# Kernel tuning notes

Hardware: AMD Instinct MI355X
Metric: run time of the kernel (lower is better)

Reference implementation:

```python
import jax, jax.numpy as jnp
import numpy as np

EPS = 1e-5


def setup_inputs() -> dict:
    key = jax.random.key(0)
    k1, k2, k3, k4 = jax.random.split(key, 4)
    N, E, D = 100000, 1600000, 128
    x = jax.random.normal(k1, (N, D), dtype=jnp.float32)
    weight = jax.random.normal(k2, (D, D), dtype=jnp.float32) * (1.0 / np.sqrt(D))
    bias = jnp.zeros((D,), dtype=jnp.float32)
    src = jax.random.randint(k3, (E,), 0, N, dtype=jnp.int32)
    dst = jax.random.randint(k4, (E,), 0, N, dtype=jnp.int32)
    return {"x": x, "weight": weight, "bias": bias, "src": src, "dst": dst}


def reference(x, weight, bias, src, dst):
    # GNNBasicBlock(layer_type='gcn', block_type='n_a_r', activation=('relu', False))
    N = x.shape[0]
    ones = jnp.ones(src.shape[0], dtype=x.dtype)
    # DGL GraphConv norm='both': D_out^{-1/2} on src side, D_in^{-1/2} on dst side,
    # degrees clamped to min 1.
    out_deg = jax.ops.segment_sum(ones, src, num_segments=N)
    in_deg = jax.ops.segment_sum(ones, dst, num_segments=N)
    norm_src = jnp.maximum(out_deg, 1.0) ** -0.5  # [N]
    norm_dst = jnp.maximum(in_deg, 1.0) ** -0.5   # [N]
    xs = x * norm_src[:, None]                    # [N, D]
    # gather src features per edge, sum-scatter to dst (aggregate first: in<=out)
    agg = jax.ops.segment_sum(xs[src], dst, num_segments=N)  # [E,D] -> [N,D]
    agg = agg * norm_dst[:, None]
    h = agg @ weight + bias                       # [N, D]
    # NodeNorm: per-node mean/var over feature dim, biased variance
    mean = jnp.mean(h, axis=1, keepdims=True)
    var = jnp.var(h, axis=1, keepdims=True)
    h = (h - mean) / jnp.sqrt(var + EPS)
    # relu + residual
    return jax.nn.relu(h) + x
```

## Files before the change

### kernel.cpp

```cpp
#include <hip/hip_runtime.h>

#define D 128
#define SPAN 64
#define NB_MAX 1600
#define CB 128
#define ECAP 1536

typedef __attribute__((ext_vector_type(8))) short short8;
typedef __attribute__((ext_vector_type(4))) float floatx4;
typedef __attribute__((ext_vector_type(4))) int   iv4;
typedef __attribute__((ext_vector_type(4))) float fv4;

__device__ __forceinline__ short f32_bf16(float f) {
    unsigned u = __builtin_bit_cast(unsigned, f);
    u += 0x7fffu + ((u >> 16) & 1u);
    return (short)(u >> 16);
}

__device__ __forceinline__ iv4 nt4i(const int* p) {
    return __builtin_nontemporal_load((const iv4*)p);
}
__device__ __forceinline__ fv4 nt4f(const float* p) {
    return __builtin_nontemporal_load((const fv4*)p);
}


__global__ __launch_bounds__(256) void k_count(const int* __restrict__ dst,
                                               int* __restrict__ counts,
                                               int E, int NB, int V4) {
    __shared__ int cl[NB_MAX];
    const int tid = threadIdx.x;
    const int b = blockIdx.x;
    for (int i = tid; i < NB; i += 256) cl[i] = 0;
    __syncthreads();
    const int nv4 = E >> 2;
    const int v0 = b * V4;
    const int v1 = min(v0 + V4, nv4);
    for (int v = v0 + tid; v < v1; v += 256) {
        iv4 d = nt4i(dst + 4 * v);
        atomicAdd(&cl[d[0] >> 6], 1);
        atomicAdd(&cl[d[1] >> 6], 1);
        atomicAdd(&cl[d[2] >> 6], 1);
        atomicAdd(&cl[d[3] >> 6], 1);
    }
    if (b == CB - 1) {
        for (int e = (nv4 << 2) + tid; e < E; e += 256)
            atomicAdd(&cl[dst[e] >> 6], 1);
    }
    __syncthreads();
    for (int i = tid; i < NB; i += 256) counts[b * NB + i] = cl[i];
}

__global__ __launch_bounds__(256) void k_scanA(int* __restrict__ counts,
                                               int* __restrict__ btot,
                                               int NB) {
    __shared__ int s[CB];
    const int tid = threadIdx.x;
    const int b = blockIdx.x;
    int mine = 0;
    if (tid < CB) { mine = counts[tid * NB + b]; s[tid] = mine; }
    __syncthreads();
    for (int off = 1; off < CB; off <<= 1) {
        int t = 0;
        if (tid < CB && tid >= off) t = s[tid - off];
        __syncthreads();
        if (tid < CB) s[tid] += t;
        __syncthreads();
    }
    if (tid < CB) counts[tid * NB + b] = s[tid] - mine;
    if (tid == CB - 1) btot[b] = s[CB - 1];
}

__global__ __launch_bounds__(256) void k_scanB(const int* __restrict__ btot,
                                               int* __restrict__ bbase,
                                               int NB) {
    __shared__ int s[256];
    __shared__ int carry_s;
    const int tid = threadIdx.x;
    if (tid == 0) carry_s = 0;
    __syncthreads();
    for (int base = 0; base < NB; base += 256) {
        const int ccur = carry_s;
        int v = (base + tid < NB) ? btot[base + tid] : 0;
        const int mine = v;
        s[tid] = v;
        __syncthreads();
        for (int off = 1; off < 256; off <<= 1) {
            int t = (tid >= off) ? s[tid - off] : 0;
            __syncthreads();
            s[tid] += t;
            __syncthreads();
        }
        if (base + tid < NB) bbase[base + tid] = ccur + s[tid] - mine;
        const int tot = s[255];
        __syncthreads();
        if (tid == 0) carry_s = ccur + tot;
        __syncthreads();
    }
}

__global__ __launch_bounds__(256) void k_hist_out(const int* __restrict__ src,
                                                  int* __restrict__ outdeg,
                                                  int E) {
    const int t = blockIdx.x * 256 + threadIdx.x;
    const int nv = E >> 2;
    if (t < nv) {
        iv4 s = nt4i(src + 4 * t);
        atomicAdd(&outdeg[s[0]], 1);
        atomicAdd(&outdeg[s[1]], 1);
        atomicAdd(&outdeg[s[2]], 1);
        atomicAdd(&outdeg[s[3]], 1);
    }
    int e = (nv << 2) + t;
    if (e < E) atomicAdd(&outdeg[src[e]], 1);
}

__global__ __launch_bounds__(256) void k_cvt(const float* __restrict__ x,
                                             const int* __restrict__ outdeg,
                                             unsigned short* __restrict__ xb,
                                             int ng) {
    int i = blockIdx.x * 256 + threadIdx.x;
    if (i >= ng) return;
    int r = i >> 4;
    float ns = rsqrtf((float)max(outdeg[r], 1));
    fv4 a = nt4f(x + 8 * (size_t)i);
    fv4 b = nt4f(x + 8 * (size_t)i + 4);
    short8 v;
    v[0] = f32_bf16(a[0] * ns); v[1] = f32_bf16(a[1] * ns);
    v[2] = f32_bf16(a[2] * ns); v[3] = f32_bf16(a[3] * ns);
    v[4] = f32_bf16(b[0] * ns); v[5] = f32_bf16(b[1] * ns);
    v[6] = f32_bf16(b[2] * ns); v[7] = f32_bf16(b[3] * ns);
    *(short8*)(xb + (size_t)i * 8) = v;
}

__global__ __launch_bounds__(256) void k_norm(const int* __restrict__ outdeg,
                                              float* __restrict__ nsrc, int N) {
    int i = blockIdx.x * 256 + threadIdx.x;
    if (i < N) nsrc[i] = rsqrtf((float)max(outdeg[i], 1));
}

__global__ __launch_bounds__(256) void k_binscat(const int* __restrict__ src,
                                                 const int* __restrict__ dst,
                                                 const int* __restrict__ counts,
                                                 const int* __restrict__ bbase,
                                                 unsigned* __restrict__ ebuf,
                                                 int E, int NB, int V4) {
    __shared__ int pos[NB_MAX];
    const int tid = threadIdx.x;
    const int b = blockIdx.x;
    for (int i = tid; i < NB; i += 256) pos[i] = bbase[i] + counts[b * NB + i];
    __syncthreads();
    const int nv4 = E >> 2;
    const int v0 = b * V4;
    const int v1 = min(v0 + V4, nv4);
    for (int v = v0 + tid; v < v1; v += 256) {
        iv4 d = nt4i(dst + 4 * v);
        iv4 s = nt4i(src + 4 * v);
        #pragma unroll
        for (int k = 0; k < 4; ++k) {
            int p = atomicAdd(&pos[d[k] >> 6], 1);
            ebuf[p] = ((unsigned)s[k] << 6) | (unsigned)(d[k] & 63);
        }
    }
    if (b == CB - 1) {
        for (int e = (nv4 << 2) + tid; e < E; e += 256) {
            int dd = dst[e];
            int p = atomicAdd(&pos[dd >> 6], 1);
            ebuf[p] = ((unsigned)src[e] << 6) | (unsigned)(dd & 63);
        }
    }
}

template<bool BF>
__global__ __launch_bounds__(256) void k_aggs(const unsigned* __restrict__ ebuf,
                                              const int* __restrict__ bbase,
                                              const int* __restrict__ btot,
                                              const unsigned* __restrict__ xb,
                                              const float* __restrict__ x,
                                              const float* __restrict__ nsrc,
                                              float* __restrict__ agg, int N) {
    __shared__ int cntl[SPAN];
    __shared__ int startl[SPAN + 1];
    __shared__ int offl[SPAN];
    __shared__ unsigned ids[ECAP];
    const int tid = threadIdx.x;
    const int b = blockIdx.x;
    const int e0 = bbase[b];
    const int cap = min(btot[b], ECAP);

    if (tid < SPAN) cntl[tid] = 0;
    __syncthreads();
    for (int i = tid; i < cap; i += 256)
        atomicAdd(&cntl[ebuf[e0 + i] & 63], 1);
    __syncthreads();
    if (tid == 0) {
        int o = 0;
        #pragma unroll
        for (int k = 0; k < SPAN; ++k) { startl[k] = o; o += cntl[k]; }
        startl[SPAN] = o;
    }
    __syncthreads();
    if (tid < SPAN) offl[tid] = startl[tid];
    __syncthreads();
    for (int i = tid; i < cap; i += 256) {
        unsigned u = ebuf[e0 + i];
        int p = atomicAdd(&offl[u & 63], 1);
        ids[p] = u >> 6;
    }
    __syncthreads();

    const int w = tid >> 6;
    const int lane = tid & 63;
    for (int j = 0; j < 16; ++j) {
        const int dl = w * 16 + j;
        const int c = cntl[dl];
        const int bs = startl[dl];
        const int g = b * SPAN + dl;
        float ax = 0.f, ay = 0.f;
        if (BF) {
            int i = 0;
            for (; i + 4 <= c; i += 4) {
                int s0 = ids[bs + i];
                int s1 = ids[bs + i + 1];
                int s2 = ids[bs + i + 2];
                int s3 = ids[bs + i + 3];
                unsigned u0 = xb[(size_t)s0 * 64 + lane];
                unsigned u1 = xb[(size_t)s1 * 64 + lane];
                unsigned u2 = xb[(size_t)s2 * 64 + lane];
                unsigned u3 = xb[(size_t)s3 * 64 + lane];
                ax += __builtin_bit_cast(float, u0 << 16);
                ay += __builtin_bit_cast(float, u0 & 0xffff0000u);
                ax += __builtin_bit_cast(float, u1 << 16);
                ay += __builtin_bit_cast(float, u1 & 0xffff0000u);
                ax += __builtin_bit_cast(float, u2 << 16);
                ay += __builtin_bit_cast(float, u2 & 0xffff0000u);
                ax += __builtin_bit_cast(float, u3 << 16);
                ay += __builtin_bit_cast(float, u3 & 0xffff0000u);
            }
            for (; i < c; ++i) {
                unsigned u0 = xb[(size_t)ids[bs + i] * 64 + lane];
                ax += __builtin_bit_cast(float, u0 << 16);
                ay += __builtin_bit_cast(float, u0 & 0xffff0000u);
            }
        } else {
            const float2* __restrict__ x2 = (const float2*)x;
            int i = 0;
            for (; i + 4 <= c; i += 4) {
                int s0 = ids[bs + i];
                int s1 = ids[bs + i + 1];
                int s2 = ids[bs + i + 2];
                int s3 = ids[bs + i + 3];
                float a0 = nsrc[s0], a1 = nsrc[s1], a2 = nsrc[s2], a3 = nsrc[s3];
                float2 v0 = x2[(size_t)s0 * 64 + lane];
                float2 v1 = x2[(size_t)s1 * 64 + lane];
                float2 v2 = x2[(size_t)s2 * 64 + lane];
                float2 v3 = x2[(size_t)s3 * 64 + lane];
                ax = fmaf(v0.x, a0, ax); ay = fmaf(v0.y, a0, ay);
                ax = fmaf(v1.x, a1, ax); ay = fmaf(v1.y, a1, ay);
                ax = fmaf(v2.x, a2, ax); ay = fmaf(v2.y, a2, ay);
                ax = fmaf(v3.x, a3, ax); ay = fmaf(v3.y, a3, ay);
            }
            for (; i < c; ++i) {
                int s0 = ids[bs + i];
                float a0 = nsrc[s0];
                float2 v0 = x2[(size_t)s0 * 64 + lane];
                ax = fmaf(v0.x, a0, ax); ay = fmaf(v0.y, a0, ay);
            }
        }
        if (g < N) {
            float nd = rsqrtf((float)max(c, 1));
            ((float2*)agg)[(size_t)g * 64 + lane] = make_float2(ax * nd, ay * nd);
        }
    }
}

#define WT_STRIDE 136
#define H_STRIDE  132

__global__ __launch_bounds__(256, 2) void k_gemm_norm(
    const float* __restrict__ agg,
    const float* __restrict__ x,
    const float* __restrict__ W,
    const float* __restrict__ bias,
    float* __restrict__ out, int N)
{
    __shared__ char raw[D * WT_STRIDE * 2];
    short* Wt = (short*)raw;
    float* h  = (float*)raw;

    const int t = threadIdx.x;
    const int lane = t & 63;
    const int w = t >> 6;
    const int row0 = blockIdx.x * 64;

    #pragma unroll 4
    for (int i = 0; i < 64; ++i) {
        int idx = t + i * 256;
        int k = idx >> 7, c = idx & 127;
        Wt[c * WT_STRIDE + k] = f32_bf16(W[idx]);
    }
    __syncthreads();

    const int col16 = lane & 15;
    const int quad  = lane >> 4;
    int arow = row0 + w * 16 + col16;
    if (arow >= N) arow = N - 1;
    const float* aptr = agg + (long long)arow * D + quad * 8;

    floatx4 acc[8];
    #pragma unroll
    for (int c = 0; c < 8; ++c) {
        float b = bias[c * 16 + col16];
        acc[c] = (floatx4){b, b, b, b};
    }

    #pragma unroll
    for (int kc = 0; kc < 4; ++kc) {
        float4 a0 = *(const float4*)(aptr + kc * 32);
        float4 a1 = *(const float4*)(aptr + kc * 32 + 4);
        short8 af;
        af[0] = f32_bf16(a0.x); af[1] = f32_bf16(a0.y);
        af[2] = f32_bf16(a0.z); af[3] = f32_bf16(a0.w);
        af[4] = f32_bf16(a1.x); af[5] = f32_bf16(a1.y);
        af[6] = f32_bf16(a1.z); af[7] = f32_bf16(a1.w);
        const short* wbase = Wt + kc * 32 + quad * 8;
        #pragma unroll
        for (int c = 0; c < 8; ++c) {
            short8 bf = *(const short8*)(wbase + (c * 16 + col16) * WT_STRIDE);
            acc[c] = __builtin_amdgcn_mfma_f32_16x16x32_bf16(af, bf, acc[c], 0, 0, 0);
        }
    }
    __syncthreads();

    #pragma unroll
    for (int c = 0; c < 8; ++c) {
        #pragma unroll
        for (int i = 0; i < 4; ++i) {
            h[(w * 16 + quad * 4 + i) * H_STRIDE + c * 16 + col16] = acc[c][i];
        }
    }
    __syncthreads();

    const int row = t >> 2;
    const int part = t & 3;
    const float* hp = h + row * H_STRIDE + part * 32;
    float4 hv[8];
    float s = 0.f, ss = 0.f;
    #pragma unroll
    for (int i = 0; i < 8; ++i) {
        float4 v = *(const float4*)(hp + i * 4);
        hv[i] = v;
        s  += v.x + v.y + v.z + v.w;
        ss += v.x * v.x + v.y * v.y + v.z * v.z + v.w * v.w;
    }
    s += __shfl_xor(s, 1); ss += __shfl_xor(ss, 1);
    s += __shfl_xor(s, 2); ss += __shfl_xor(ss, 2);
    const float mean = s * (1.0f / 128.0f);
    const float var = ss * (1.0f / 128.0f) - mean * mean;
    const float inv = rsqrtf(var + 1e-5f);
    const int grow = row0 + row;
    if (grow < N) {
        const float* xp = x + (long long)grow * D + part * 32;
        float* op = out + (long long)grow * D + part * 32;
        #pragma unroll
        for (int i = 0; i < 8; ++i) {
            float4 v = hv[i];
            float4 xr = *(const float4*)(xp + i * 4);
            float4 o;
            o.x = fmaxf((v.x - mean) * inv, 0.f) + xr.x;
            o.y = fmaxf((v.y - mean) * inv, 0.f) + xr.y;
            o.z = fmaxf((v.z - mean) * inv, 0.f) + xr.z;
            o.w = fmaxf((v.w - mean) * inv, 0.f) + xr.w;
            *(float4*)(op + i * 4) = o;
        }
    }
}

extern "C" void kernel_launch(void* const* d_in, const int* in_sizes, int n_in,
                              void* d_out, int out_size, void* d_ws, size_t ws_size,
                              hipStream_t stream) {
    const float* x    = (const float*)d_in[0];
    const float* W    = (const float*)d_in[1];
    const float* bias = (const float*)d_in[2];
    const int*   src  = (const int*)d_in[3];
    const int*   dst  = (const int*)d_in[4];
    const int N = in_sizes[0] / D;
    const int E = in_sizes[3];
    float* out = (float*)d_out;

    const int NB = (N + SPAN - 1) / SPAN;

    auto al = [](size_t b) { return (b + 255) & ~(size_t)255; };
    size_t outdeg_b = al((size_t)N * 4);
    size_t counts_b = al((size_t)CB * NB * 4);
    size_t btot_b   = al((size_t)NB * 4);
    size_t bbase_b  = al((size_t)NB * 4);
    size_t nsrc_b   = al((size_t)N * 4);
    size_t ebuf_b   = al((size_t)E * 4);
    size_t xb_b     = al((size_t)N * D * 2);

    size_t need_core = outdeg_b + counts_b + btot_b + bbase_b + nsrc_b + ebuf_b;
    bool use_bf = (ws_size >= need_core + xb_b);

    char* p = (char*)d_ws;
    int*      outdeg = (int*)p;      p += outdeg_b;
    int*      counts = (int*)p;      p += counts_b;
    int*      btot   = (int*)p;      p += btot_b;
    int*      bbase  = (int*)p;      p += bbase_b;
    float*    nsrc   = (float*)p;    p += nsrc_b;
    unsigned* ebuf   = (unsigned*)p; p += ebuf_b;
    unsigned short* xb = (unsigned short*)p;

    float* agg = out;

    hipMemsetAsync(outdeg, 0, outdeg_b, stream);

    const int nv4 = E >> 2;
    const int V4  = (nv4 + CB - 1) / CB;
    const int EB4 = (nv4 + 255) / 256 + 1;
    const int NBLK = (N + 255) / 256;

    k_count  <<<CB, 256, 0, stream>>>(dst, counts, E, NB, V4);
    k_scanA  <<<NB, 256, 0, stream>>>(counts, btot, NB);
    k_scanB  <<<1, 256, 0, stream>>>(btot, bbase, NB);
    k_hist_out<<<EB4, 256, 0, stream>>>(src, outdeg, E);
    if (use_bf) {
        int ng = N * 16;
        k_cvt<<<(ng + 255) / 256, 256, 0, stream>>>(x, outdeg, xb, ng);
    } else {
        k_norm<<<NBLK, 256, 0, stream>>>(outdeg, nsrc, N);
    }
    k_binscat<<<CB, 256, 0, stream>>>(src, dst, counts, bbase, ebuf, E, NB, V4);
    if (use_bf) {
        k_aggs<true><<<NB, 256, 0, stream>>>(ebuf, bbase, btot,
                                             (const unsigned*)xb, x, nsrc, agg, N);
    } else {
        k_aggs<false><<<NB, 256, 0, stream>>>(ebuf, bbase, btot,
                                              nullptr, x, nsrc, agg, N);
    }
    k_gemm_norm<<<(N + 63) / 64, 256, 0, stream>>>(agg, x, W, bias, out, N);
}
```

Before: 345.3 us.

## Compute out-degrees via binned src counting instead of global atomic histogram

Replaces the global-memory atomic out-degree histogram with a second binning pass over src: counts per 64-node src bin in the same count kernel, bins src low bits into a new buffer during scatter, then counts per-bin in LDS to produce norm_src. The two scan kernels are merged into one, using a last-block-done counter to run the cross-bin prefix for both D and S. This removes roughly 1.6M contended global atomics and a kernel launch, but adds an extra E-sized write and read, doubled LDS atomics in count/scatter, and makes the bf16 conversion wait until after scatter.

```diff
diff --git a/kernel.cpp b/kernel.cpp
--- a/kernel.cpp
+++ b/kernel.cpp
@@ -25,40 +25,62 @@
 }
 
 
-__global__ __launch_bounds__(256) void k_count(const int* __restrict__ dst,
-                                               int* __restrict__ counts,
-                                               int E, int NB, int V4) {
-    __shared__ int cl[NB_MAX];
+__global__ __launch_bounds__(256) void k_count2(const int* __restrict__ src,
+                                                const int* __restrict__ dst,
+                                                int* __restrict__ countsD,
+                                                int* __restrict__ countsS,
+                                                int E, int NB, int V4) {
+    __shared__ int cld[NB_MAX];
+    __shared__ int cls[NB_MAX];
     const int tid = threadIdx.x;
     const int b = blockIdx.x;
-    for (int i = tid; i < NB; i += 256) cl[i] = 0;
+    for (int i = tid; i < NB; i += 256) { cld[i] = 0; cls[i] = 0; }
     __syncthreads();
     const int nv4 = E >> 2;
     const int v0 = b * V4;
     const int v1 = min(v0 + V4, nv4);
     for (int v = v0 + tid; v < v1; v += 256) {
         iv4 d = nt4i(dst + 4 * v);
-        atomicAdd(&cl[d[0] >> 6], 1);
-        atomicAdd(&cl[d[1] >> 6], 1);
-        atomicAdd(&cl[d[2] >> 6], 1);
-        atomicAdd(&cl[d[3] >> 6], 1);
+        iv4 s = nt4i(src + 4 * v);
+        #pragma unroll
+        for (int k = 0; k < 4; ++k) {
+            atomicAdd(&cld[d[k] >> 6], 1);
+            atomicAdd(&cls[s[k] >> 6], 1);
+        }
     }
     if (b == CB - 1) {
-        for (int e = (nv4 << 2) + tid; e < E; e += 256)
-            atomicAdd(&cl[dst[e] >> 6], 1);
-    }
-    __syncthreads();
-    for (int i = tid; i < NB; i += 256) counts[b * NB + i] = cl[i];
-}
-
-__global__ __launch_bounds__(256) void k_scanA(int* __restrict__ counts,
-                                               int* __restrict__ btot,
+        for (int e = (nv4 << 2) + tid; e < E; e += 256) {
+            atomicAdd(&cld[dst[e] >> 6], 1);
+            atomicAdd(&cls[src[e] >> 6], 1);
+        }
+    }
+    __syncthreads();
+    for (int i = tid; i < NB; i += 256) {
+        countsD[b * NB + i] = cld[i];
+        countsS[b * NB + i] = cls[i];
+    }
+}
+
+__global__ __launch_bounds__(256) void k_scan2(int* __restrict__ countsD,
+                                               int* __restrict__ countsS,
+                                               int* __restrict__ btotD,
+                                               int* __restrict__ btotS,
+                                               int* __restrict__ bbaseD,
+                                               int* __restrict__ bbaseS,
+                                               int* __restrict__ done,
                                                int NB) {
-    __shared__ int s[CB];
+    __shared__ int s[256];
+    __shared__ int lastflag;
+    __shared__ int carry;
     const int tid = threadIdx.x;
     const int b = blockIdx.x;
+    const bool isD = (b < NB);
+    const int bk = isD ? b : b - NB;
+    int* counts = isD ? countsD : countsS;
+    int* btot   = isD ? btotD  : btotS;
+
     int mine = 0;
-    if (tid < CB) { mine = counts[tid * NB + b]; s[tid] = mine; }
+    if (tid < CB) { mine = counts[tid * NB + bk]; s[tid] = mine; }
     __syncthreads();
     for (int off = 1; off < CB; off <<= 1) {
         int t = 0;
@@ -67,62 +89,119 @@
         if (tid < CB) s[tid] += t;
         __syncthreads();
     }
-    if (tid < CB) counts[tid * NB + b] = s[tid] - mine;
-    if (tid == CB - 1) btot[b] = s[CB - 1];
-}
-
-__global__ __launch_bounds__(256) void k_scanB(const int* __restrict__ btot,
-                                               int* __restrict__ bbase,
-                                               int NB) {
-    __shared__ int s[256];
-    __shared__ int carry_s;
+    if (tid < CB) counts[tid * NB + bk] = s[tid] - mine;
+    if (tid == CB - 1)
+        __hip_atomic_store(&btot[bk], s[CB - 1], __ATOMIC_RELEASE,
+                           __HIP_MEMORY_SCOPE_AGENT);
+    __syncthreads();
+    if (tid == 0) {
+        int old = __hip_atomic_fetch_add(done, 1, __ATOMIC_ACQ_REL,
+                                         __HIP_MEMORY_SCOPE_AGENT);
+        lastflag = (old == (int)gridDim.x - 1);
+    }
+    __syncthreads();
+    if (!lastflag) return;
+
+    for (int pass = 0; pass < 2; ++pass) {
+        const int* bt = pass ? btotS : btotD;
+        int* bb = pass ? bbaseS : bbaseD;
+        if (tid == 0) carry = 0;
+        __syncthreads();
+        for (int base = 0; base < NB; base += 256) {
+            const int ccur = carry;
+            int v = 0;
+            if (base + tid < NB)
+                v = __hip_atomic_load(&bt[base + tid], __ATOMIC_RELAXED,
+                                      __HIP_MEMORY_SCOPE_AGENT);
+            const int mn = v;
+            s[tid] = v;
+            __syncthreads();
+            for (int off = 1; off < 256; off <<= 1) {
+                int t = (tid >= off) ? s[tid - off] : 0;
+                __syncthreads();
+                s[tid] += t;
+                __syncthreads();
+            }
+            if (base + tid < NB) bb[base + tid] = ccur + s[tid] - mn;
+            const int tot = s[255];
+            __syncthreads();
+            if (tid == 0) carry = ccur + tot;
+            __syncthreads();
+        }
+    }
+}
+
+__global__ __launch_bounds__(256) void k_binscat2(const int* __restrict__ src,
+                                                  const int* __restrict__ dst,
+                                                  const int* __restrict__ countsD,
+                                                  const int* __restrict__ countsS,
+                                                  const int* __restrict__ bbaseD,
+                                                  const int* __restrict__ bbaseS,
+                                                  unsigned* __restrict__ ebuf,
+                                                  unsigned* __restrict__ sbuf,
+                                                  int E, int NB, int V4) {
+    __shared__ int posD[NB_MAX];
+    __shared__ int posS[NB_MAX];
     const int tid = threadIdx.x;
-    if (tid == 0) carry_s = 0;
-    __syncthreads();
-    for (int base = 0; base < NB; base += 256) {
-        const int ccur = carry_s;
-        int v = (base + tid < NB) ? btot[base + tid] : 0;
-        const int mine = v;
-        s[tid] = v;
-        __syncthreads();
-        for (int off = 1; off < 256; off <<= 1) {
-            int t = (tid >= off) ? s[tid - off] : 0;
-            __syncthreads();
-            s[tid] += t;
-            __syncthreads();
-        }
-        if (base + tid < NB) bbase[base + tid] = ccur + s[tid] - mine;
-        const int tot = s[255];
-        __syncthreads();
-        if (tid == 0) carry_s = ccur + tot;
-        __syncthreads();
-    }
-}
-
-__global__ __launch_bounds__(256) void k_hist_out(const int* __restrict__ src,
-                                                  int* __restrict__ outdeg,
-                                                  int E) {
-    const int t = blockIdx.x * 256 + threadIdx.x;
-    const int nv = E >> 2;
-    if (t < nv) {
-        iv4 s = nt4i(src + 4 * t);
-        atomicAdd(&outdeg[s[0]], 1);
-        atomicAdd(&outdeg[s[1]], 1);
-        atomicAdd(&outdeg[s[2]], 1);
-        atomicAdd(&outdeg[s[3]], 1);
-    }
-    int e = (nv << 2) + t;
-    if (e < E) atomicAdd(&outdeg[src[e]], 1);
+    const int b = blockIdx.x;
+    for (int i = tid; i < NB; i += 256) {
+        posD[i] = bbaseD[i] + countsD[b * NB + i];
+        posS[i] = bbaseS[i] + countsS[b * NB + i];
+    }
+    __syncthreads();
+    const int nv4 = E >> 2;
+    const int v0 = b * V4;
+    const int v1 = min(v0 + V4, nv4);
+    for (int v = v0 + tid; v < v1; v += 256) {
+        iv4 d = nt4i(dst + 4 * v);
+        iv4 s = nt4i(src + 4 * v);
+        #pragma unroll
+        for (int k = 0; k < 4; ++k) {
+            int pD = atomicAdd(&posD[d[k] >> 6], 1);
+            ebuf[pD] = ((unsigned)s[k] << 6) | (unsigned)(d[k] & 63);
+            int pS = atomicAdd(&posS[s[k] >> 6], 1);
+            sbuf[pS] = (unsigned)(s[k] & 63);
+        }
+    }
+    if (b == CB - 1) {
+        for (int e = (nv4 << 2) + tid; e < E; e += 256) {
+            int dd = dst[e], ss = src[e];
+            int pD = atomicAdd(&posD[dd >> 6], 1);
+            ebuf[pD] = ((unsigned)ss << 6) | (unsigned)(dd & 63);
+            int pS = atomicAdd(&posS[ss >> 6], 1);
+            sbuf[pS] = (unsigned)(ss & 63);
+        }
+    }
+}
+
+__global__ __launch_bounds__(256) void k_odeg(const unsigned* __restrict__ sbuf,
+                                              const int* __restrict__ bbaseS,
+                                              const int* __restrict__ btotS,
+                                              float* __restrict__ nsrc, int N) {
+    __shared__ int cl[SPAN];
+    const int tid = threadIdx.x;
+    const int b = blockIdx.x;
+    if (tid < SPAN) cl[tid] = 0;
+    __syncthreads();
+    const int e0 = bbaseS[b];
+    const int c = btotS[b];
+    for (int i = tid; i < c; i += 256)
+        atomicAdd(&cl[sbuf[e0 + i] & 63], 1);
+    __syncthreads();
+    if (tid < SPAN) {
+        int g = b * SPAN + tid;
+        if (g < N) nsrc[g] = rsqrtf((float)max(cl[tid], 1));
+    }
 }
 
 __global__ __launch_bounds__(256) void k_cvt(const float* __restrict__ x,
-                                             const int* __restrict__ outdeg,
+                                             const float* __restrict__ nsrc,
                                              unsigned short* __restrict__ xb,
                                              int ng) {
     int i = blockIdx.x * 256 + threadIdx.x;
     if (i >= ng) return;
     int r = i >> 4;
-    float ns = rsqrtf((float)max(outdeg[r], 1));
+    float ns = nsrc[r];
     fv4 a = nt4f(x + 8 * (size_t)i);
     fv4 b = nt4f(x + 8 * (size_t)i + 4);
     short8 v;
@@ -131,44 +210,6 @@
     v[4] = f32_bf16(b[0] * ns); v[5] = f32_bf16(b[1] * ns);
     v[6] = f32_bf16(b[2] * ns); v[7] = f32_bf16(b[3] * ns);
     *(short8*)(xb + (size_t)i * 8) = v;
-}
-
-__global__ __launch_bounds__(256) void k_norm(const int* __restrict__ outdeg,
-                                              float* __restrict__ nsrc, int N) {
-    int i = blockIdx.x * 256 + threadIdx.x;
-    if (i < N) nsrc[i] = rsqrtf((float)max(outdeg[i], 1));
-}
-
-__global__ __launch_bounds__(256) void k_binscat(const int* __restrict__ src,
-                                                 const int* __restrict__ dst,
-                                                 const int* __restrict__ counts,
-                                                 const int* __restrict__ bbase,
-                                                 unsigned* __restrict__ ebuf,
-                                                 int E, int NB, int V4) {
-    __shared__ int pos[NB_MAX];
-    const int tid = threadIdx.x;
-    const int b = blockIdx.x;
-    for (int i = tid; i < NB; i += 256) pos[i] = bbase[i] + counts[b * NB + i];
-    __syncthreads();
-    const int nv4 = E >> 2;
-    const int v0 = b * V4;
-    const int v1 = min(v0 + V4, nv4);
-    for (int v = v0 + tid; v < v1; v += 256) {
-        iv4 d = nt4i(dst + 4 * v);
-        iv4 s = nt4i(src + 4 * v);
-        #pragma unroll
-        for (int k = 0; k < 4; ++k) {
-            int p = atomicAdd(&pos[d[k] >> 6], 1);
-            ebuf[p] = ((unsigned)s[k] << 6) | (unsigned)(d[k] & 63);
-        }
-    }
-    if (b == CB - 1) {
-        for (int e = (nv4 << 2) + tid; e < E; e += 256) {
-            int dd = dst[e];
-            int p = atomicAdd(&pos[dd >> 6], 1);
-            ebuf[p] = ((unsigned)src[e] << 6) | (unsigned)(dd & 63);
-        }
-    }
 }
 
 template<bool BF>
@@ -391,51 +432,52 @@
     const int NB = (N + SPAN - 1) / SPAN;
 
     auto al = [](size_t b) { return (b + 255) & ~(size_t)255; };
-    size_t outdeg_b = al((size_t)N * 4);
-    size_t counts_b = al((size_t)CB * NB * 4);
-    size_t btot_b   = al((size_t)NB * 4);
-    size_t bbase_b  = al((size_t)NB * 4);
-    size_t nsrc_b   = al((size_t)N * 4);
-    size_t ebuf_b   = al((size_t)E * 4);
-    size_t xb_b     = al((size_t)N * D * 2);
-
-    size_t need_core = outdeg_b + counts_b + btot_b + bbase_b + nsrc_b + ebuf_b;
+    size_t countsD_b = al((size_t)CB * NB * 4);
+    size_t countsS_b = al((size_t)CB * NB * 4);
+    size_t btot_b    = al((size_t)NB * 4);
+    size_t nsrc_b    = al((size_t)N * 4);
+    size_t ebuf_b    = al((size_t)E * 4);
+    size_t sbuf_b    = al((size_t)E * 4);
+    size_t ctrl_b    = 256;
+    size_t xb_b      = al((size_t)N * D * 2);
+
+    size_t need_core = countsD_b + countsS_b + 4 * btot_b + nsrc_b +
+                       ebuf_b + sbuf_b + ctrl_b;
     bool use_bf = (ws_size >= need_core + xb_b);
 
     char* p = (char*)d_ws;
-    int*      outdeg = (int*)p;      p += outdeg_b;
-    int*      counts = (int*)p;      p += counts_b;
-    int*      btot   = (int*)p;      p += btot_b;
-    int*      bbase  = (int*)p;      p += bbase_b;
-    float*    nsrc   = (float*)p;    p += nsrc_b;
-    unsigned* ebuf   = (unsigned*)p; p += ebuf_b;
+    int*      countsD = (int*)p;     p += countsD_b;
+    int*      countsS = (int*)p;     p += countsS_b;
+    int*      btotD   = (int*)p;     p += btot_b;
+    int*      btotS   = (int*)p;     p += btot_b;
+    int*      bbaseD  = (int*)p;     p += btot_b;
+    int*      bbaseS  = (int*)p;     p += btot_b;
+    float*    nsrc    = (float*)p;   p += nsrc_b;
+    unsigned* ebuf    = (unsigned*)p; p += ebuf_b;
+    unsigned* sbuf    = (unsigned*)p; p += sbuf_b;
+    int*      done    = (int*)p;     p += ctrl_b;
     unsigned short* xb = (unsigned short*)p;
 
     float* agg = out;
 
-    hipMemsetAsync(outdeg, 0, outdeg_b, stream);
+    hipMemsetAsync(done, 0, 64, stream);
 
     const int nv4 = E >> 2;
     const int V4  = (nv4 + CB - 1) / CB;
-    const int EB4 = (nv4 + 255) / 256 + 1;
-    const int NBLK = (N + 255) / 256;
-
-    k_count  <<<CB, 256, 0, stream>>>(dst, counts, E, NB, V4);
-    k_scanA  <<<NB, 256, 0, stream>>>(counts, btot, NB);
-    k_scanB  <<<1, 256, 0, stream>>>(btot, bbase, NB);
-    k_hist_out<<<EB4, 256, 0, stream>>>(src, outdeg, E);
+
+    k_count2  <<<CB, 256, 0, stream>>>(src, dst, countsD, countsS, E, NB, V4);
+    k_scan2   <<<2 * NB, 256, 0, stream>>>(countsD, countsS, btotD, btotS,
+                                           bbaseD, bbaseS, done, NB);
+    k_binscat2<<<CB, 256, 0, stream>>>(src, dst, countsD, countsS,
+                                       bbaseD, bbaseS, ebuf, sbuf, E, NB, V4);
+    k_odeg    <<<NB, 256, 0, stream>>>(sbuf, bbaseS, btotS, nsrc, N);
     if (use_bf) {
         int ng = N * 16;
-        k_cvt<<<(ng + 255) / 256, 256, 0, stream>>>(x, outdeg, xb, ng);
-    } else {
-        k_norm<<<NBLK, 256, 0, stream>>>(outdeg, nsrc, N);
-    }
-    k_binscat<<<CB, 256, 0, stream>>>(src, dst, counts, bbase, ebuf, E, NB, V4);
-    if (use_bf) {
-        k_aggs<true><<<NB, 256, 0, stream>>>(ebuf, bbase, btot,
+        k_cvt<<<(ng + 255) / 256, 256, 0, stream>>>(x, nsrc, xb, ng);
+        k_aggs<true><<<NB, 256, 0, stream>>>(ebuf, bbaseD, btotD,
                                              (const unsigned*)xb, x, nsrc, agg, N);
     } else {
-        k_aggs<false><<<NB, 256, 0, stream>>>(ebuf, bbase, btot,
+        k_aggs<false><<<NB, 256, 0, stream>>>(ebuf, bbaseD, btotD,
                                               nullptr, x, nsrc, agg, N);
     }
     k_gemm_norm<<<(N + 63) / 64, 256, 0, stream>>>(agg, x, W, bias, out, N);
```

Measured after the change: 477.4 us. 1.38x slower.
